# Kernel optimization log

Measured on AMD Instinct MI355X. Metric: run time of the kernel, lower is better.

Reference implementation:

```python
import jax, jax.numpy as jnp
import numpy as np

EPS = 1e-8

def setup_inputs() -> dict:
    key = jax.random.key(0)
    kz, ky = jax.random.split(key)
    Z = jax.random.normal(kz, (4096, 4096), dtype=jnp.float32)
    Y = jax.random.normal(ky, (4096, 4096), dtype=jnp.float32)
    return {"Z": Z, "Y": Y}

def reference(Z, Y):
    # Flatten per-sample features (matches Z.reshape(B, -1))
    x = Z.reshape(Z.shape[0], -1)
    y = Y.reshape(Y.shape[0], -1)
    # Pairwise cosine similarity: single GEMM + outer norm product,
    # replacing the O(Bz*By) Python double loop.
    dots = x @ y.T                                   # [Bz, By]
    nx = jnp.linalg.norm(x, axis=1)                  # [Bz]
    ny = jnp.linalg.norm(y, axis=1)                  # [By]
    denom = jnp.maximum(nx[:, None] * ny[None, :], EPS)
    similarity = dots / denom
    return similarity
```

## Files before the change

### kernel.cpp

```cpp
#include <hip/hip_runtime.h>

typedef __attribute__((ext_vector_type(4))) int i32x4;

#define N 4096

__global__ __launch_bounds__(256) void prep_kernel(
    const float* __restrict__ Z, const float* __restrict__ Y,
    char* __restrict__ Zq, char* __restrict__ Yq,
    float* __restrict__ norms, float* __restrict__ scales) {
  const int r = blockIdx.x;
  const bool isZ = (r < N);
  const int rr = isZ ? r : r - N;
  const float* __restrict__ src = (isZ ? Z : Y) + (size_t)rr * N;
  char* __restrict__ dst = (isZ ? Zq : Yq) + (size_t)rr * N;
  const int t = threadIdx.x;

  float4 v[4];
  float s = 0.f, amax = 0.f;
#pragma unroll
  for (int j = 0; j < 4; ++j) {
    v[j] = ((const float4*)src)[t * 4 + j];
    s += v[j].x * v[j].x + v[j].y * v[j].y + v[j].z * v[j].z + v[j].w * v[j].w;
    amax = fmaxf(amax, fmaxf(fmaxf(fabsf(v[j].x), fabsf(v[j].y)),
                             fmaxf(fabsf(v[j].z), fabsf(v[j].w))));
  }
#pragma unroll
  for (int off = 32; off > 0; off >>= 1) {
    s += __shfl_down(s, off, 64);
    amax = fmaxf(amax, __shfl_down(amax, off, 64));
  }
  __shared__ float reds[4], redm[4];
  const int lane = t & 63, w = t >> 6;
  if (lane == 0) { reds[w] = s; redm[w] = amax; }
  __syncthreads();
  const float bmax = fmaxf(fmaxf(redm[0], redm[1]), fmaxf(redm[2], redm[3]));
  if (t == 0) {
    norms[r] = sqrtf(reds[0] + reds[1] + reds[2] + reds[3]);
    scales[r] = bmax * (1.0f / 127.0f);
  }
  const float inv = (bmax > 0.f) ? (127.0f / bmax) : 0.f;
  int q[16];
#pragma unroll
  for (int j = 0; j < 4; ++j) {
    q[4 * j + 0] = __float2int_rn(v[j].x * inv);
    q[4 * j + 1] = __float2int_rn(v[j].y * inv);
    q[4 * j + 2] = __float2int_rn(v[j].z * inv);
    q[4 * j + 3] = __float2int_rn(v[j].w * inv);
  }
  int4 o;
  o.x = (q[0] & 255) | ((q[1] & 255) << 8) | ((q[2] & 255) << 16) | (q[3] << 24);
  o.y = (q[4] & 255) | ((q[5] & 255) << 8) | ((q[6] & 255) << 16) | (q[7] << 24);
  o.z = (q[8] & 255) | ((q[9] & 255) << 8) | ((q[10] & 255) << 16) | (q[11] << 24);
  o.w = (q[12] & 255) | ((q[13] & 255) << 8) | ((q[14] & 255) << 16) | (q[15] << 24);
  ((int4*)dst)[t] = o;
}

__global__ __launch_bounds__(512, 2) void gemm_kernel(
    const char* __restrict__ A,
    const char* __restrict__ B,
    const float* __restrict__ norms,
    const float* __restrict__ scales,
    float* __restrict__ out) {
  __shared__ __align__(16) char smem[131072];

  const int bid = blockIdx.x;
  const int swz = (bid & 7) * 32 + (bid >> 3);
  const int tile_row = swz >> 4;
  const int tile_col = swz & 15;

  const int tid = threadIdx.x;
  const int l = tid & 63;
  const int w = tid >> 6;
  const int wr = w >> 2;
  const int wc = w & 3;
  const int li = l & 15;
  const int sl = l >> 4;

  const char *pA00, *pA01, *pA10, *pA11, *pB00, *pB01, *pB10, *pB11;
  {
    const int ch0 = tid, ch1 = 512 + tid;
    const int r0 = ch0 >> 3, r1 = ch1 >> 3;
    const int c0 = ((ch0 & 7) ^ (r0 & 7)) * 16;
    const int c1 = ((ch1 & 7) ^ (r1 & 7)) * 16;
    pA00 = A + (size_t)(tile_row * 256 + r0) * N + c0;
    pA01 = A + (size_t)(tile_row * 256 + r1) * N + c1;
    pA10 = A + (size_t)(tile_row * 256 + 128 + r0) * N + c0;
    pA11 = A + (size_t)(tile_row * 256 + 128 + r1) * N + c1;
    pB00 = B + (size_t)(tile_col * 256 + r0) * N + c0;
    pB01 = B + (size_t)(tile_col * 256 + r1) * N + c1;
    pB10 = B + (size_t)(tile_col * 256 + 128 + r0) * N + c0;
    pB11 = B + (size_t)(tile_col * 256 + 128 + r1) * N + c1;
  }

#define GLD(SRC, DST)                                              \
  __builtin_amdgcn_global_load_lds(                                \
      (__attribute__((address_space(1))) void*)(SRC),              \
      (__attribute__((address_space(3))) void*)(DST), 16, 0, 0)
#define STG(REGOFF, P0, P1, KOFF) {                                \
    GLD((P0) + (KOFF), smem + (REGOFF) + w * 1024);                \
    GLD((P1) + (KOFF), smem + (REGOFF) + 8192 + w * 1024); }

  const int rbA = (wr * 64 + li) * 128;
  const int rbB = (wc * 32 + li) * 128;
  const int sx0 = ((sl) ^ (li & 7)) * 16;
  const int sx1 = ((4 + sl) ^ (li & 7)) * 16;

  i32x4 aC[4][2], bQ0[2][2], bQ1[2][2];
  i32x4 acc[8][4];
#pragma unroll
  for (int m = 0; m < 8; ++m)
#pragma unroll
    for (int n = 0; n < 4; ++n) acc[m][n] = (i32x4){0, 0, 0, 0};

#define RD_A(BUFB, QH) { _Pragma("unroll")                                    \
    for (int mfl = 0; mfl < 4; ++mfl) {                                       \
      aC[mfl][0] = *(const i32x4*)(smem + (BUFB) + (QH)*16384 + rbA +         \
                                   mfl*2048 + sx0);                           \
      aC[mfl][1] = *(const i32x4*)(smem + (BUFB) + (QH)*16384 + rbA +         \
                                   mfl*2048 + sx1); } }
#define RD_B(DST, BUFB, QH) { _Pragma("unroll")                               \
    for (int nfl = 0; nfl < 2; ++nfl) {                                       \
      DST[nfl][0] = *(const i32x4*)(smem + (BUFB) + 32768 + (QH)*16384 +      \
                                    rbB + nfl*2048 + sx0);                    \
      DST[nfl][1] = *(const i32x4*)(smem + (BUFB) + 32768 + (QH)*16384 +      \
                                    rbB + nfl*2048 + sx1); } }

#define MFQ(QM, QN, BF) {                                                     \
    __builtin_amdgcn_s_setprio(1);                                            \
    _Pragma("unroll") for (int kh = 0; kh < 2; ++kh)                          \
    _Pragma("unroll") for (int mfl = 0; mfl < 4; ++mfl)                       \
    _Pragma("unroll") for (int nfl = 0; nfl < 2; ++nfl)                       \
      acc[(QM)*4+mfl][(QN)*2+nfl] = __builtin_amdgcn_mfma_i32_16x16x64_i8(    \
          aC[mfl][kh], BF[nfl][kh], acc[(QM)*4+mfl][(QN)*2+nfl], 0, 0, 0);    \
    __builtin_amdgcn_s_setprio(0); }

#define SB   __builtin_amdgcn_sched_barrier(0);
#define BAR  __builtin_amdgcn_s_barrier();
#define VMW2 asm volatile("s_waitcnt vmcnt(2)" ::: "memory");
#define VMW4 asm volatile("s_waitcnt vmcnt(4)" ::: "memory");
#define VMW0 asm volatile("s_waitcnt vmcnt(0)" ::: "memory");
#define LGW4 { asm volatile("s_waitcnt lgkmcnt(4)" ::: "memory"); SB }
#define LGW0 { asm volatile("s_waitcnt lgkmcnt(0)" ::: "memory"); SB }

  STG(0, pA00, pA01, 0);
  STG(32768, pB00, pB01, 0);
  STG(49152, pB10, pB11, 0);
  STG(16384, pA10, pA11, 0);
  VMW4; BAR; SB;
  RD_A(0, 0); RD_B(bQ0, 0, 0);

#pragma unroll 1
  for (int k = 0; k < 15; ++k) {
    VMW2; BAR; SB;
    RD_B(bQ1, 0, 1);
    STG(65536, pA00, pA01, 128);
    LGW4;
    MFQ(0, 0, bQ0);
    VMW2; BAR;
    STG(98304, pB00, pB01, 128);
    LGW0;
    MFQ(0, 1, bQ1);
    SB;
    RD_A(0, 1);
    BAR;
    STG(114688, pB10, pB11, 128);
    LGW0;
    MFQ(1, 1, bQ1);
    VMW2; BAR;
    STG(81920, pA10, pA11, 128);
    MFQ(1, 0, bQ0);
    SB;
    RD_A(65536, 0); RD_B(bQ0, 65536, 0);
    VMW2; BAR; SB;
    RD_B(bQ1, 65536, 1);
    STG(0, pA00, pA01, 256);
    LGW4;
    MFQ(0, 0, bQ0);
    VMW2; BAR;
    STG(32768, pB00, pB01, 256);
    LGW0;
    MFQ(0, 1, bQ1);
    SB;
    RD_A(65536, 1);
    BAR;
    STG(49152, pB10, pB11, 256);
    LGW0;
    MFQ(1, 1, bQ1);
    VMW2; BAR;
    STG(16384, pA10, pA11, 256);
    MFQ(1, 0, bQ0);
    SB;
    RD_A(0, 0); RD_B(bQ0, 0, 0);
    pA00 += 256; pA01 += 256; pA10 += 256; pA11 += 256;
    pB00 += 256; pB01 += 256; pB10 += 256; pB11 += 256;
  }

  VMW2; BAR; SB;
  RD_B(bQ1, 0, 1);
  STG(65536, pA00, pA01, 128);
  LGW4;
  MFQ(0, 0, bQ0);
  VMW2; BAR;
  STG(98304, pB00, pB01, 128);
  LGW0;
  MFQ(0, 1, bQ1);
  SB;
  RD_A(0, 1);
  BAR;
  STG(114688, pB10, pB11, 128);
  LGW0;
  MFQ(1, 1, bQ1);
  VMW2; BAR;
  STG(81920, pA10, pA11, 128);
  MFQ(1, 0, bQ0);
  SB;
  RD_A(65536, 0); RD_B(bQ0, 65536, 0);
  VMW2; BAR; SB;
  RD_B(bQ1, 65536, 1);
  LGW4;
  MFQ(0, 0, bQ0);
  VMW0; BAR;
  LGW0;
  MFQ(0, 1, bQ1);
  SB;
  RD_A(65536, 1);
  LGW0;
  MFQ(1, 1, bQ1);
  MFQ(1, 0, bQ0);

  const float* nx = norms;
  const float* ny = norms + N;
  const float* sxp = scales;
  const float* syp = scales + N;
#pragma unroll
  for (int mf = 0; mf < 8; ++mf) {
#pragma unroll
    for (int r = 0; r < 4; ++r) {
      const int row = tile_row * 256 + (mf >> 2) * 128 + wr * 64 +
                      (mf & 3) * 16 + sl * 4 + r;
      const float nxr = nx[row];
      const float sxr = sxp[row];
#pragma unroll
      for (int nf = 0; nf < 4; ++nf) {
        const int col = tile_col * 256 + (nf >> 1) * 128 + wc * 32 +
                        (nf & 1) * 16 + li;
        const float denom = fmaxf(nxr * ny[col], 1e-8f);
        out[(size_t)row * N + col] =
            (float)acc[mf][nf][r] * (sxr * syp[col]) / denom;
      }
    }
  }
}

extern "C" void kernel_launch(void* const* d_in, const int* in_sizes, int n_in,
                              void* d_out, int out_size, void* d_ws, size_t ws_size,
                              hipStream_t stream) {
  const float* Z = (const float*)d_in[0];
  const float* Y = (const float*)d_in[1];
  float* out = (float*)d_out;

  char* Zq = (char*)d_ws;
  char* Yq = Zq + (size_t)N * N;
  float* norms = (float*)(Yq + (size_t)N * N);
  float* scales = norms + 2 * N;

  prep_kernel<<<2 * N, 256, 0, stream>>>(Z, Y, Zq, Yq, norms, scales);
  gemm_kernel<<<(N / 256) * (N / 256), 512, 0, stream>>>(Zq, Yq, norms, scales,
                                                         out);
}
```

Measured before the change: 90.38 us.

## Switch int8 GEMM from 16x16x64 to 32x32x32 MFMA with new LDS swizzle

Replaces the 16x16x64 i8 MFMA tiling with 32x32x32 i8 MFMA instructions. Each wave now computes 2x2 blocks of 32x32 per quadrant, so it issues fewer MFMAs and fewer LDS fragment reads for the same tile. The LDS XOR swizzle gains an extra term to avoid bank conflicts under the new 32-lane row access pattern, and the epilogue is remapped to the 32x32 accumulator layout. Accumulators stay at the same register count, but the instruction latency and scheduling characteristics change.

```diff
diff --git a/kernel.cpp b/kernel.cpp
--- a/kernel.cpp
+++ b/kernel.cpp
@@ -1,6 +1,7 @@
 #include <hip/hip_runtime.h>
 
 typedef __attribute__((ext_vector_type(4))) int i32x4;
+typedef __attribute__((ext_vector_type(16))) int i32x16;
 
 #define N 4096
 
@@ -73,15 +74,15 @@
   const int w = tid >> 6;
   const int wr = w >> 2;
   const int wc = w & 3;
-  const int li = l & 15;
-  const int sl = l >> 4;
+  const int l31 = l & 31;
+  const int kh = l >> 5;
 
   const char *pA00, *pA01, *pA10, *pA11, *pB00, *pB01, *pB10, *pB11;
   {
     const int ch0 = tid, ch1 = 512 + tid;
     const int r0 = ch0 >> 3, r1 = ch1 >> 3;
-    const int c0 = ((ch0 & 7) ^ (r0 & 7)) * 16;
-    const int c1 = ((ch1 & 7) ^ (r1 & 7)) * 16;
+    const int c0 = ((ch0 & 7) ^ (r0 & 7) ^ ((r0 >> 3) & 3)) * 16;
+    const int c1 = ((ch1 & 7) ^ (r1 & 7) ^ ((r1 >> 3) & 3)) * 16;
     pA00 = A + (size_t)(tile_row * 256 + r0) * N + c0;
     pA01 = A + (size_t)(tile_row * 256 + r1) * N + c1;
     pA10 = A + (size_t)(tile_row * 256 + 128 + r0) * N + c0;
@@ -100,38 +101,39 @@
     GLD((P0) + (KOFF), smem + (REGOFF) + w * 1024);                \
     GLD((P1) + (KOFF), smem + (REGOFF) + 8192 + w * 1024); }
 
-  const int rbA = (wr * 64 + li) * 128;
-  const int rbB = (wc * 32 + li) * 128;
-  const int sx0 = ((sl) ^ (li & 7)) * 16;
-  const int sx1 = ((4 + sl) ^ (li & 7)) * 16;
-
-  i32x4 aC[4][2], bQ0[2][2], bQ1[2][2];
-  i32x4 acc[8][4];
-#pragma unroll
-  for (int m = 0; m < 8; ++m)
-#pragma unroll
-    for (int n = 0; n < 4; ++n) acc[m][n] = (i32x4){0, 0, 0, 0};
-
-#define RD_A(BUFB, QH) { _Pragma("unroll")                                    \
-    for (int mfl = 0; mfl < 4; ++mfl) {                                       \
-      aC[mfl][0] = *(const i32x4*)(smem + (BUFB) + (QH)*16384 + rbA +         \
-                                   mfl*2048 + sx0);                           \
-      aC[mfl][1] = *(const i32x4*)(smem + (BUFB) + (QH)*16384 + rbA +         \
-                                   mfl*2048 + sx1); } }
-#define RD_B(DST, BUFB, QH) { _Pragma("unroll")                               \
-    for (int nfl = 0; nfl < 2; ++nfl) {                                       \
-      DST[nfl][0] = *(const i32x4*)(smem + (BUFB) + 32768 + (QH)*16384 +      \
-                                    rbB + nfl*2048 + sx0);                    \
-      DST[nfl][1] = *(const i32x4*)(smem + (BUFB) + 32768 + (QH)*16384 +      \
-                                    rbB + nfl*2048 + sx1); } }
+  const int fl = (l31 & 7) ^ ((l31 >> 3) & 3);
+  const int rbA = (wr * 64 + l31) * 128;
+  const int rbB = 32768 + (wc * 32 + l31) * 128;
+  int sxk[4];
+#pragma unroll
+  for (int ks = 0; ks < 4; ++ks) sxk[ks] = (((ks << 1) + kh) ^ fl) << 4;
+
+  i32x4 aC[2][4], bQ0[4], bQ1[4];
+  i32x16 acc[2][2][2];
+#pragma unroll
+  for (int qm = 0; qm < 2; ++qm)
+#pragma unroll
+    for (int mf = 0; mf < 2; ++mf)
+#pragma unroll
+      for (int qn = 0; qn < 2; ++qn)
+#pragma unroll
+        for (int rg = 0; rg < 16; ++rg) acc[qm][mf][qn][rg] = 0;
+
+#define RD_A(BUFB, QM) { _Pragma("unroll")                                    \
+    for (int mf = 0; mf < 2; ++mf)                                            \
+    _Pragma("unroll") for (int ks = 0; ks < 4; ++ks)                          \
+      aC[mf][ks] = *(const i32x4*)(smem + (BUFB) + (QM)*16384 + rbA +         \
+                                   mf*4096 + sxk[ks]); }
+#define RD_B(DST, BUFB, QN) { _Pragma("unroll")                               \
+    for (int ks = 0; ks < 4; ++ks)                                            \
+      DST[ks] = *(const i32x4*)(smem + (BUFB) + (QN)*16384 + rbB + sxk[ks]); }
 
 #define MFQ(QM, QN, BF) {                                                     \
     __builtin_amdgcn_s_setprio(1);                                            \
-    _Pragma("unroll") for (int kh = 0; kh < 2; ++kh)                          \
-    _Pragma("unroll") for (int mfl = 0; mfl < 4; ++mfl)                       \
-    _Pragma("unroll") for (int nfl = 0; nfl < 2; ++nfl)                       \
-      acc[(QM)*4+mfl][(QN)*2+nfl] = __builtin_amdgcn_mfma_i32_16x16x64_i8(    \
-          aC[mfl][kh], BF[nfl][kh], acc[(QM)*4+mfl][(QN)*2+nfl], 0, 0, 0);    \
+    _Pragma("unroll") for (int ks = 0; ks < 4; ++ks)                          \
+    _Pragma("unroll") for (int mf = 0; mf < 2; ++mf)                          \
+      acc[QM][mf][QN] = __builtin_amdgcn_mfma_i32_32x32x32_i8(                \
+          aC[mf][ks], BF[ks], acc[QM][mf][QN], 0, 0, 0);                      \
     __builtin_amdgcn_s_setprio(0); }
 
 #define SB   __builtin_amdgcn_sched_barrier(0);
@@ -233,20 +235,25 @@
   const float* sxp = scales;
   const float* syp = scales + N;
 #pragma unroll
-  for (int mf = 0; mf < 8; ++mf) {
-#pragma unroll
-    for (int r = 0; r < 4; ++r) {
-      const int row = tile_row * 256 + (mf >> 2) * 128 + wr * 64 +
-                      (mf & 3) * 16 + sl * 4 + r;
-      const float nxr = nx[row];
-      const float sxr = sxp[row];
-#pragma unroll
-      for (int nf = 0; nf < 4; ++nf) {
-        const int col = tile_col * 256 + (nf >> 1) * 128 + wc * 32 +
-                        (nf & 1) * 16 + li;
-        const float denom = fmaxf(nxr * ny[col], 1e-8f);
-        out[(size_t)row * N + col] =
-            (float)acc[mf][nf][r] * (sxr * syp[col]) / denom;
+  for (int qm = 0; qm < 2; ++qm) {
+#pragma unroll
+    for (int mf = 0; mf < 2; ++mf) {
+#pragma unroll
+      for (int rg = 0; rg < 4; ++rg) {
+#pragma unroll
+        for (int rr = 0; rr < 4; ++rr) {
+          const int row = tile_row * 256 + qm * 128 + wr * 64 + mf * 32 +
+                          rg * 8 + rr + 4 * kh;
+          const float nxr = nx[row];
+          const float sxr = sxp[row];
+#pragma unroll
+          for (int qn = 0; qn < 2; ++qn) {
+            const int col = tile_col * 256 + qn * 128 + wc * 32 + l31;
+            const float denom = fmaxf(nxr * ny[col], 1e-8f);
+            out[(size_t)row * N + col] =
+                (float)acc[qm][mf][qn][rg * 4 + rr] * (sxr * syp[col]) / denom;
+          }
+        }
       }
     }
   }
```

Result: slower. 99.75 us (+10.4%).
